# Performance work log

Measured on AMD Instinct MI355X. Metric: run time of the kernel, lower is better.

Reference implementation:

```python
import jax, jax.numpy as jnp
import numpy as np

B, S, D, N, R = 4, 2048, 1024, 64, 128

def setup_inputs() -> dict:
    key = jax.random.key(0)
    k1, k2, k3, k4, k5 = jax.random.split(key, 5)
    x = jax.random.normal(k1, (B, S, D), dtype=jnp.float32)
    feature_know_w = jax.random.uniform(k2, (B, S, N), dtype=jnp.float32)
    restore_know_w = jax.random.uniform(k3, (B, S, N), dtype=jnp.float32)
    # neuron pools, scaled like typical init
    feature_know = jax.random.normal(k4, (N, D, R), dtype=jnp.float32) / np.sqrt(D)
    restore_know = jax.random.normal(k5, (N, R, D), dtype=jnp.float32) / np.sqrt(R)
    return {"x": x, "feature_know_w": feature_know_w, "restore_know_w": restore_know_w,
            "feature_know": feature_know, "restore_know": restore_know}

def reference(x, feature_know_w, restore_know_w, feature_know, restore_know):
    # Feature stage: all_h[b,s,n,r] = sum_d x[b,s,d] * feature_know[n,d,r];
    # h[b,s,r] = sum_n all_h[b,s,n,r] * feature_know_w[b,s,n].
    # Fused into one einsum (same math, XLA picks pairwise contraction;
    # largest intermediate is [B,S,N,R], never [B,S,N,D]).
    h = jnp.einsum('bsd,ndr,bsn->bsr', x, feature_know, feature_know_w)
    # Restore stage: all_out[b,s,n,d] = sum_r h[b,s,r] * restore_know[n,r,d];
    # out[b,s,d] = sum_n all_out[b,s,n,d] * restore_know_w[b,s,n].
    # Reordered contraction keeps the intermediate at [B,S,N,R] instead of [B,S,N,D].
    out = jnp.einsum('bsr,bsn,nrd->bsd', h, restore_know_w, restore_know)
    # dropout p=0.0 -> identity
    return out
```

## Files before the change

### kernel.cpp

```cpp
#include <hip/hip_runtime.h>
#include <stdint.h>


typedef unsigned short ushort_t;
typedef __attribute__((ext_vector_type(8))) short frag_t;
typedef __attribute__((ext_vector_type(4))) float f32x4;

#define BK 128

__device__ __forceinline__ unsigned short f2bf(float f) {
    unsigned int u = __builtin_bit_cast(unsigned int, f);
    u = (u + 0x7FFFu + ((u >> 16) & 1u)) >> 16;
    return (unsigned short)u;
}

__device__ __forceinline__ void glds16(const ushort_t* g, ushort_t* l) {
    __builtin_amdgcn_global_load_lds(
        (const __attribute__((address_space(1))) unsigned int*)g,
        (__attribute__((address_space(3))) unsigned int*)l,
        16, 0, 0);
}

__global__ __launch_bounds__(256) void convert_bf(const float* __restrict__ in,
                                                  ushort_t* __restrict__ out, int n8) {
    int idx = blockIdx.x * 256 + threadIdx.x;
    if (idx >= n8) return;
    const float4 v0 = ((const float4*)in)[idx * 2];
    const float4 v1 = ((const float4*)in)[idx * 2 + 1];
    unsigned short b[8] = { f2bf(v0.x), f2bf(v0.y), f2bf(v0.z), f2bf(v0.w),
                            f2bf(v1.x), f2bf(v1.y), f2bf(v1.z), f2bf(v1.w) };
    ((uint4*)out)[idx] = *(const uint4*)b;
}

__global__ __launch_bounds__(256) void transpose_bf(const float* __restrict__ in,
                                                    ushort_t* __restrict__ out,
                                                    int R, int C) {
    __shared__ float tile[64][65];
    const int t  = threadIdx.x;
    const int r0 = blockIdx.x * 64;
    const int c0 = blockIdx.y * 64;
    const int ci = t & 63;
    const int rb = t >> 6;
    #pragma unroll
    for (int p = 0; p < 16; ++p)
        tile[rb + 4 * p][ci] = in[(size_t)(r0 + rb + 4 * p) * C + c0 + ci];
    __syncthreads();
    const int cw = t >> 2;
    const int rg = (t & 3) * 16;
    unsigned short buf[16];
    #pragma unroll
    for (int k = 0; k < 16; ++k)
        buf[k] = f2bf(tile[rg + k][cw]);
    uint4* dst = (uint4*)&out[(size_t)(c0 + cw) * R + r0 + rg];
    dst[0] = *(const uint4*)&buf[0];
    dst[1] = *(const uint4*)&buf[8];
}

template<int SHIFT, int SEG_STEPS, bool ATOMIC>
__global__ __launch_bounds__(256, 2)
void kc_gemm(const ushort_t* __restrict__ Ab, const float* __restrict__ W,
             const ushort_t* __restrict__ Bt, float* __restrict__ C,
             int ldA, int ldB, int ldC, int ksteps)
{
    __shared__ ushort_t As[128 * BK];
    __shared__ ushort_t Bs[128 * BK];

    const int t    = threadIdx.x;
    const int lane = t & 63;
    const int wv   = t >> 6;
    const int m0   = blockIdx.x * 128;
    const int n0   = blockIdx.y * 128;
    const int kbase = blockIdx.z * ksteps * BK;

    const int wm = (wv & 1) * 64;
    const int wn = (wv >> 1) * 64;
    const int fr = lane & 15;
    const int q  = lane >> 4;

    int srow[8], scol[8];
    #pragma unroll
    for (int c = 0; c < 8; ++c) {
        const int s = (wv * 8 + c) * 64 + lane;
        srow[c] = s >> 4;
        scol[c] = ((s & 15) ^ (srow[c] & 15)) * 8;
    }

    f32x4 acc_out[4][4], acc_in[4][4];
    #pragma unroll
    for (int i = 0; i < 4; ++i)
        #pragma unroll
        for (int j = 0; j < 4; ++j)
            acc_out[i][j] = (f32x4){0.f, 0.f, 0.f, 0.f};

    const int nsegs = ksteps / SEG_STEPS;
    for (int seg = 0; seg < nsegs; ++seg) {
        const int segk = kbase + seg * SEG_STEPS * BK;
        const int nidx = segk >> SHIFT;

        #pragma unroll
        for (int i = 0; i < 4; ++i)
            #pragma unroll
            for (int j = 0; j < 4; ++j)
                acc_in[i][j] = (f32x4){0.f, 0.f, 0.f, 0.f};

        for (int ss = 0; ss < SEG_STEPS; ++ss) {
            const int k0 = segk + ss * BK;
            const int d0 = k0 & ((1 << SHIFT) - 1);

            __syncthreads();
            #pragma unroll
            for (int c = 0; c < 8; ++c) {
                glds16(Ab + (size_t)(m0 + srow[c]) * ldA + d0 + scol[c],
                       &As[(wv * 8 + c) * 512]);
                glds16(Bt + (size_t)(n0 + srow[c]) * ldB + k0 + scol[c],
                       &Bs[(wv * 8 + c) * 512]);
            }
            __syncthreads();

            #pragma unroll
            for (int kk = 0; kk < 4; ++kk) {
                frag_t a[4], b[4];
                const int csw = (q + 4 * kk) ^ fr;
                #pragma unroll
                for (int i = 0; i < 4; ++i) {
                    a[i] = *(const frag_t*)&As[((wm + 16 * i + fr) * 16 + csw) * 8];
                    b[i] = *(const frag_t*)&Bs[((wn + 16 * i + fr) * 16 + csw) * 8];
                }
                #pragma unroll
                for (int i = 0; i < 4; ++i)
                    #pragma unroll
                    for (int j = 0; j < 4; ++j)
                        acc_in[i][j] = __builtin_amdgcn_mfma_f32_16x16x32_bf16(
                                           a[i], b[j], acc_in[i][j], 0, 0, 0);
            }
        }

        #pragma unroll
        for (int i = 0; i < 4; ++i) {
            #pragma unroll
            for (int r = 0; r < 4; ++r) {
                const int gm = m0 + wm + 16 * i + q * 4 + r;
                const float w = W[(size_t)gm * 64 + nidx];
                #pragma unroll
                for (int j = 0; j < 4; ++j)
                    acc_out[i][j][r] += w * acc_in[i][j][r];
            }
        }
    }

    #pragma unroll
    for (int i = 0; i < 4; ++i) {
        #pragma unroll
        for (int j = 0; j < 4; ++j) {
            #pragma unroll
            for (int r = 0; r < 4; ++r) {
                const int gm = m0 + wm + 16 * i + q * 4 + r;
                const int gn = n0 + wn + 16 * j + fr;
                if constexpr (ATOMIC)
                    atomicAdd(&C[(size_t)gm * ldC + gn], acc_out[i][j][r]);
                else
                    C[(size_t)gm * ldC + gn] = acc_out[i][j][r];
            }
        }
    }
}

extern "C" void kernel_launch(void* const* d_in, const int* in_sizes, int n_in,
                              void* d_out, int out_size, void* d_ws, size_t ws_size,
                              hipStream_t stream) {
    const float* x  = (const float*)d_in[0];
    const float* w1 = (const float*)d_in[1];
    const float* w2 = (const float*)d_in[2];
    const float* F  = (const float*)d_in[3];
    const float* Rk = (const float*)d_in[4];
    float* out = (float*)d_out;

    char* ws = (char*)d_ws;
    float*    h    = (float*)ws;
    ushort_t* buf1 = (ushort_t*)(ws + ((size_t)4  << 20));
    ushort_t* F_t  = (ushort_t*)(ws + ((size_t)20 << 20));
    ushort_t* h_bf = (ushort_t*)(ws + ((size_t)36 << 20));

    hipMemsetAsync(h, 0, (size_t)8192 * 128 * sizeof(float), stream);

    convert_bf<<<4096, 256, 0, stream>>>(x, buf1, 1048576);
    transpose_bf<<<dim3(1024, 2), 256, 0, stream>>>(F, F_t, 65536, 128);

    kc_gemm<10, 8, true><<<dim3(64, 1, 8), 256, 0, stream>>>(
        buf1, w1, F_t, h, 1024, 65536, 128, 64);

    convert_bf<<<512, 256, 0, stream>>>(h, h_bf, 131072);
    transpose_bf<<<dim3(128, 16), 256, 0, stream>>>(Rk, buf1, 8192, 1024);

    kc_gemm<7, 1, false><<<dim3(64, 8, 1), 256, 0, stream>>>(
        h_bf, w2, buf1, out, 128, 8192, 1024, 64);
}
```

Before: 497.0 us.

## Shrink GEMM tile to 64x128 with BK=64 to raise occupancy and block count

Shrinks the GEMM block tile from 128x128 with BK=128 to 64x128 with BK=64. LDS shrinks and per-wave accumulators halve, so the launch bound rises to 4 blocks per CU. The grids double in the M dimension and the K-step and segment counts are rescaled to match, with a new XOR swizzle for the 8-chunk rows. The goal is more resident waves and more blocks to hide latency across the CUs. In exchange, each tile reuses its loads less, adds more barrier round-trips per unit of work, and the feature GEMM issues more atomics.

```diff
diff --git a/kernel.cpp b/kernel.cpp
--- a/kernel.cpp
+++ b/kernel.cpp
@@ -6,7 +6,7 @@
 typedef __attribute__((ext_vector_type(8))) short frag_t;
 typedef __attribute__((ext_vector_type(4))) float f32x4;
 
-#define BK 128
+#define BK 64
 
 __device__ __forceinline__ unsigned short f2bf(float f) {
     unsigned int u = __builtin_bit_cast(unsigned int, f);
@@ -57,37 +57,45 @@
 }
 
 template<int SHIFT, int SEG_STEPS, bool ATOMIC>
-__global__ __launch_bounds__(256, 2)
+__global__ __launch_bounds__(256, 4)
 void kc_gemm(const ushort_t* __restrict__ Ab, const float* __restrict__ W,
              const ushort_t* __restrict__ Bt, float* __restrict__ C,
              int ldA, int ldB, int ldC, int ksteps)
 {
-    __shared__ ushort_t As[128 * BK];
+    __shared__ ushort_t As[64 * BK];
     __shared__ ushort_t Bs[128 * BK];
 
     const int t    = threadIdx.x;
     const int lane = t & 63;
     const int wv   = t >> 6;
-    const int m0   = blockIdx.x * 128;
+    const int m0   = blockIdx.x * 64;
     const int n0   = blockIdx.y * 128;
     const int kbase = blockIdx.z * ksteps * BK;
 
-    const int wm = (wv & 1) * 64;
+    const int wm = (wv & 1) * 32;
     const int wn = (wv >> 1) * 64;
     const int fr = lane & 15;
     const int q  = lane >> 4;
-
-    int srow[8], scol[8];
-    #pragma unroll
-    for (int c = 0; c < 8; ++c) {
-        const int s = (wv * 8 + c) * 64 + lane;
-        srow[c] = s >> 4;
-        scol[c] = ((s & 15) ^ (srow[c] & 15)) * 8;
-    }
-
-    f32x4 acc_out[4][4], acc_in[4][4];
-    #pragma unroll
-    for (int i = 0; i < 4; ++i)
+    const int e  = fr & 7;
+
+    int arow[2], acol[2];
+    #pragma unroll
+    for (int c = 0; c < 2; ++c) {
+        const int s = (wv * 2 + c) * 64 + lane;
+        arow[c] = s >> 3;
+        acol[c] = ((s & 7) ^ (arow[c] & 7)) * 8;
+    }
+    int brow[4], bcol[4];
+    #pragma unroll
+    for (int c = 0; c < 4; ++c) {
+        const int s = (wv * 4 + c) * 64 + lane;
+        brow[c] = s >> 3;
+        bcol[c] = ((s & 7) ^ (brow[c] & 7)) * 8;
+    }
+
+    f32x4 acc_out[2][4];
+    #pragma unroll
+    for (int i = 0; i < 2; ++i)
         #pragma unroll
         for (int j = 0; j < 4; ++j)
             acc_out[i][j] = (f32x4){0.f, 0.f, 0.f, 0.f};
@@ -97,8 +105,9 @@
         const int segk = kbase + seg * SEG_STEPS * BK;
         const int nidx = segk >> SHIFT;
 
-        #pragma unroll
-        for (int i = 0; i < 4; ++i)
+        f32x4 acc_in[2][4];
+        #pragma unroll
+        for (int i = 0; i < 2; ++i)
             #pragma unroll
             for (int j = 0; j < 4; ++j)
                 acc_in[i][j] = (f32x4){0.f, 0.f, 0.f, 0.f};
@@ -109,25 +118,27 @@
 
             __syncthreads();
             #pragma unroll
-            for (int c = 0; c < 8; ++c) {
-                glds16(Ab + (size_t)(m0 + srow[c]) * ldA + d0 + scol[c],
-                       &As[(wv * 8 + c) * 512]);
-                glds16(Bt + (size_t)(n0 + srow[c]) * ldB + k0 + scol[c],
-                       &Bs[(wv * 8 + c) * 512]);
-            }
+            for (int c = 0; c < 2; ++c)
+                glds16(Ab + (size_t)(m0 + arow[c]) * ldA + d0 + acol[c],
+                       &As[(wv * 2 + c) * 512]);
+            #pragma unroll
+            for (int c = 0; c < 4; ++c)
+                glds16(Bt + (size_t)(n0 + brow[c]) * ldB + k0 + bcol[c],
+                       &Bs[(wv * 4 + c) * 512]);
             __syncthreads();
 
             #pragma unroll
-            for (int kk = 0; kk < 4; ++kk) {
-                frag_t a[4], b[4];
-                const int csw = (q + 4 * kk) ^ fr;
-                #pragma unroll
-                for (int i = 0; i < 4; ++i) {
-                    a[i] = *(const frag_t*)&As[((wm + 16 * i + fr) * 16 + csw) * 8];
-                    b[i] = *(const frag_t*)&Bs[((wn + 16 * i + fr) * 16 + csw) * 8];
-                }
-                #pragma unroll
-                for (int i = 0; i < 4; ++i)
+            for (int kk = 0; kk < 2; ++kk) {
+                const int csw = (kk * 4 + q) ^ e;
+                frag_t a[2], b[4];
+                #pragma unroll
+                for (int i = 0; i < 2; ++i)
+                    a[i] = *(const frag_t*)&As[((wm + 16 * i + fr) * 8 + csw) * 8];
+                #pragma unroll
+                for (int j = 0; j < 4; ++j)
+                    b[j] = *(const frag_t*)&Bs[((wn + 16 * j + fr) * 8 + csw) * 8];
+                #pragma unroll
+                for (int i = 0; i < 2; ++i)
                     #pragma unroll
                     for (int j = 0; j < 4; ++j)
                         acc_in[i][j] = __builtin_amdgcn_mfma_f32_16x16x32_bf16(
@@ -136,7 +147,7 @@
         }
 
         #pragma unroll
-        for (int i = 0; i < 4; ++i) {
+        for (int i = 0; i < 2; ++i) {
             #pragma unroll
             for (int r = 0; r < 4; ++r) {
                 const int gm = m0 + wm + 16 * i + q * 4 + r;
@@ -149,7 +160,7 @@
     }
 
     #pragma unroll
-    for (int i = 0; i < 4; ++i) {
+    for (int i = 0; i < 2; ++i) {
         #pragma unroll
         for (int j = 0; j < 4; ++j) {
             #pragma unroll
@@ -186,12 +197,12 @@
     convert_bf<<<4096, 256, 0, stream>>>(x, buf1, 1048576);
     transpose_bf<<<dim3(1024, 2), 256, 0, stream>>>(F, F_t, 65536, 128);
 
-    kc_gemm<10, 8, true><<<dim3(64, 1, 8), 256, 0, stream>>>(
-        buf1, w1, F_t, h, 1024, 65536, 128, 64);
+    kc_gemm<10, 16, true><<<dim3(128, 1, 8), 256, 0, stream>>>(
+        buf1, w1, F_t, h, 1024, 65536, 128, 128);
 
     convert_bf<<<512, 256, 0, stream>>>(h, h_bf, 131072);
     transpose_bf<<<dim3(128, 16), 256, 0, stream>>>(Rk, buf1, 8192, 1024);
 
-    kc_gemm<7, 1, false><<<dim3(64, 8, 1), 256, 0, stream>>>(
-        h_bf, w2, buf1, out, 128, 8192, 1024, 64);
-}
+    kc_gemm<7, 2, false><<<dim3(128, 8, 1), 256, 0, stream>>>(
+        h_bf, w2, buf1, out, 128, 8192, 1024, 128);
+}
```

New measurement: 500.4 us. No clear change (+0.7%).

## Split feature GEMM per neuron and pre-scale restore input into a dense g matrix

Applied to the files above, without the earlier changes.

The feature GEMM now splits across all 64 neurons in the grid z dimension. Each block scales its tile by the routing weight and atomically adds into h, replacing the in-register segment accumulation. When the workspace is large enough, a new make_g kernel writes w2-scaled h into a 8192x8192 bf16 matrix so the restore stage becomes a plain GEMM; otherwise it falls back to a per-neuron split with atomics. BK drops to 64 and the occupancy hint rises to 3. The trade is much more atomic traffic into h and a large extra g buffer written and read back, in exchange for simpler inner loops and more parallel blocks.

```diff
diff --git a/kernel.cpp b/kernel.cpp
--- a/kernel.cpp
+++ b/kernel.cpp
@@ -6,7 +6,7 @@
 typedef __attribute__((ext_vector_type(8))) short frag_t;
 typedef __attribute__((ext_vector_type(4))) float f32x4;
 
-#define BK 128
+#define BK 64
 
 __device__ __forceinline__ unsigned short f2bf(float f) {
     unsigned int u = __builtin_bit_cast(unsigned int, f);
@@ -56,11 +56,27 @@
     dst[1] = *(const uint4*)&buf[8];
 }
 
-template<int SHIFT, int SEG_STEPS, bool ATOMIC>
-__global__ __launch_bounds__(256, 2)
-void kc_gemm(const ushort_t* __restrict__ Ab, const float* __restrict__ W,
-             const ushort_t* __restrict__ Bt, float* __restrict__ C,
-             int ldA, int ldB, int ldC, int ksteps)
+__global__ __launch_bounds__(256) void make_g(const float* __restrict__ h,
+                                              const float* __restrict__ w2,
+                                              ushort_t* __restrict__ g) {
+    const int idx = blockIdx.x * 256 + threadIdx.x;
+    const int m  = idx >> 10;
+    const int c  = idx & 1023;
+    const int n  = c >> 4;
+    const int r0 = (c & 15) * 8;
+    const float w = w2[m * 64 + n];
+    const float4 h0 = *(const float4*)(h + (size_t)m * 128 + r0);
+    const float4 h1 = *(const float4*)(h + (size_t)m * 128 + r0 + 4);
+    unsigned short b[8] = { f2bf(w * h0.x), f2bf(w * h0.y), f2bf(w * h0.z), f2bf(w * h0.w),
+                            f2bf(w * h1.x), f2bf(w * h1.y), f2bf(w * h1.z), f2bf(w * h1.w) };
+    ((uint4*)g)[idx] = *(const uint4*)b;
+}
+
+template<bool SPLITN>
+__global__ __launch_bounds__(256, 3)
+void kc_gemm(const ushort_t* __restrict__ Ab, const ushort_t* __restrict__ Bt,
+             const float* __restrict__ W, float* __restrict__ C,
+             int ldA, int ldB, int ldC, int ksteps, int b_seg)
 {
     __shared__ ushort_t As[128 * BK];
     __shared__ ushort_t Bs[128 * BK];
@@ -70,96 +86,78 @@
     const int wv   = t >> 6;
     const int m0   = blockIdx.x * 128;
     const int n0   = blockIdx.y * 128;
-    const int kbase = blockIdx.z * ksteps * BK;
+    const int nz   = SPLITN ? blockIdx.z : 0;
+    const size_t bko = (size_t)nz * b_seg;
 
     const int wm = (wv & 1) * 64;
     const int wn = (wv >> 1) * 64;
     const int fr = lane & 15;
     const int q  = lane >> 4;
-
-    int srow[8], scol[8];
-    #pragma unroll
-    for (int c = 0; c < 8; ++c) {
-        const int s = (wv * 8 + c) * 64 + lane;
-        srow[c] = s >> 4;
-        scol[c] = ((s & 15) ^ (srow[c] & 15)) * 8;
-    }
-
-    f32x4 acc_out[4][4], acc_in[4][4];
+    const int e  = fr & 7;
+
+    int srow[4], scol[4];
+    #pragma unroll
+    for (int c = 0; c < 4; ++c) {
+        const int s = (wv * 4 + c) * 64 + lane;
+        srow[c] = s >> 3;
+        scol[c] = ((s & 7) ^ (srow[c] & 7)) * 8;
+    }
+
+    f32x4 acc[4][4];
     #pragma unroll
     for (int i = 0; i < 4; ++i)
         #pragma unroll
         for (int j = 0; j < 4; ++j)
-            acc_out[i][j] = (f32x4){0.f, 0.f, 0.f, 0.f};
-
-    const int nsegs = ksteps / SEG_STEPS;
-    for (int seg = 0; seg < nsegs; ++seg) {
-        const int segk = kbase + seg * SEG_STEPS * BK;
-        const int nidx = segk >> SHIFT;
-
-        #pragma unroll
-        for (int i = 0; i < 4; ++i)
+            acc[i][j] = (f32x4){0.f, 0.f, 0.f, 0.f};
+
+    for (int ss = 0; ss < ksteps; ++ss) {
+        const int k0 = ss * BK;
+
+        __syncthreads();
+        #pragma unroll
+        for (int c = 0; c < 4; ++c)
+            glds16(Ab + (size_t)(m0 + srow[c]) * ldA + k0 + scol[c],
+                   &As[(wv * 4 + c) * 512]);
+        #pragma unroll
+        for (int c = 0; c < 4; ++c)
+            glds16(Bt + (size_t)(n0 + srow[c]) * ldB + bko + k0 + scol[c],
+                   &Bs[(wv * 4 + c) * 512]);
+        __syncthreads();
+
+        #pragma unroll
+        for (int kk = 0; kk < 2; ++kk) {
+            const int csw = (kk * 4 + q) ^ e;
+            frag_t a[4], b[4];
+            #pragma unroll
+            for (int i = 0; i < 4; ++i)
+                a[i] = *(const frag_t*)&As[((wm + 16 * i + fr) * 8 + csw) * 8];
             #pragma unroll
             for (int j = 0; j < 4; ++j)
-                acc_in[i][j] = (f32x4){0.f, 0.f, 0.f, 0.f};
-
-        for (int ss = 0; ss < SEG_STEPS; ++ss) {
-            const int k0 = segk + ss * BK;
-            const int d0 = k0 & ((1 << SHIFT) - 1);
-
-            __syncthreads();
+                b[j] = *(const frag_t*)&Bs[((wn + 16 * j + fr) * 8 + csw) * 8];
             #pragma unroll
-            for (int c = 0; c < 8; ++c) {
-                glds16(Ab + (size_t)(m0 + srow[c]) * ldA + d0 + scol[c],
-                       &As[(wv * 8 + c) * 512]);
-                glds16(Bt + (size_t)(n0 + srow[c]) * ldB + k0 + scol[c],
-                       &Bs[(wv * 8 + c) * 512]);
-            }
-            __syncthreads();
-
-            #pragma unroll
-            for (int kk = 0; kk < 4; ++kk) {
-                frag_t a[4], b[4];
-                const int csw = (q + 4 * kk) ^ fr;
-                #pragma unroll
-                for (int i = 0; i < 4; ++i) {
-                    a[i] = *(const frag_t*)&As[((wm + 16 * i + fr) * 16 + csw) * 8];
-                    b[i] = *(const frag_t*)&Bs[((wn + 16 * i + fr) * 16 + csw) * 8];
-                }
-                #pragma unroll
-                for (int i = 0; i < 4; ++i)
-                    #pragma unroll
-                    for (int j = 0; j < 4; ++j)
-                        acc_in[i][j] = __builtin_amdgcn_mfma_f32_16x16x32_bf16(
-                                           a[i], b[j], acc_in[i][j], 0, 0, 0);
-            }
-        }
-
-        #pragma unroll
-        for (int i = 0; i < 4; ++i) {
-            #pragma unroll
-            for (int r = 0; r < 4; ++r) {
-                const int gm = m0 + wm + 16 * i + q * 4 + r;
-                const float w = W[(size_t)gm * 64 + nidx];
+            for (int i = 0; i < 4; ++i)
                 #pragma unroll
                 for (int j = 0; j < 4; ++j)
-                    acc_out[i][j][r] += w * acc_in[i][j][r];
-            }
+                    acc[i][j] = __builtin_amdgcn_mfma_f32_16x16x32_bf16(
+                                    a[i], b[j], acc[i][j], 0, 0, 0);
         }
     }
 
     #pragma unroll
     for (int i = 0; i < 4; ++i) {
         #pragma unroll
-        for (int j = 0; j < 4; ++j) {
-            #pragma unroll
-            for (int r = 0; r < 4; ++r) {
-                const int gm = m0 + wm + 16 * i + q * 4 + r;
-                const int gn = n0 + wn + 16 * j + fr;
-                if constexpr (ATOMIC)
-                    atomicAdd(&C[(size_t)gm * ldC + gn], acc_out[i][j][r]);
-                else
-                    C[(size_t)gm * ldC + gn] = acc_out[i][j][r];
+        for (int r = 0; r < 4; ++r) {
+            const int gm = m0 + wm + 16 * i + q * 4 + r;
+            if constexpr (SPLITN) {
+                const float w = W[(size_t)gm * 64 + nz];
+                #pragma unroll
+                for (int j = 0; j < 4; ++j)
+                    atomicAdd(&C[(size_t)gm * ldC + n0 + wn + 16 * j + fr],
+                              w * acc[i][j][r]);
+            } else {
+                #pragma unroll
+                for (int j = 0; j < 4; ++j)
+                    C[(size_t)gm * ldC + n0 + wn + 16 * j + fr] = acc[i][j][r];
             }
         }
     }
@@ -176,22 +174,46 @@
     float* out = (float*)d_out;
 
     char* ws = (char*)d_ws;
-    float*    h    = (float*)ws;
-    ushort_t* buf1 = (ushort_t*)(ws + ((size_t)4  << 20));
-    ushort_t* F_t  = (ushort_t*)(ws + ((size_t)20 << 20));
-    ushort_t* h_bf = (ushort_t*)(ws + ((size_t)36 << 20));
-
-    hipMemsetAsync(h, 0, (size_t)8192 * 128 * sizeof(float), stream);
-
-    convert_bf<<<4096, 256, 0, stream>>>(x, buf1, 1048576);
-    transpose_bf<<<dim3(1024, 2), 256, 0, stream>>>(F, F_t, 65536, 128);
-
-    kc_gemm<10, 8, true><<<dim3(64, 1, 8), 256, 0, stream>>>(
-        buf1, w1, F_t, h, 1024, 65536, 128, 64);
-
-    convert_bf<<<512, 256, 0, stream>>>(h, h_bf, 131072);
-    transpose_bf<<<dim3(128, 16), 256, 0, stream>>>(Rk, buf1, 8192, 1024);
-
-    kc_gemm<7, 1, false><<<dim3(64, 8, 1), 256, 0, stream>>>(
-        h_bf, w2, buf1, out, 128, 8192, 1024, 64);
-}
+    const size_t MB = (size_t)1 << 20;
+
+    if (ws_size >= 148 * MB) {
+        float*    h    = (float*)ws;
+        ushort_t* x_bf = (ushort_t*)(ws + 4   * MB);
+        ushort_t* F_t  = (ushort_t*)(ws + 20  * MB);
+        ushort_t* g    = (ushort_t*)(ws + 4   * MB);
+        ushort_t* Rk_t = (ushort_t*)(ws + 132 * MB);
+
+        hipMemsetAsync(h, 0, 4 * MB, stream);
+        convert_bf<<<4096, 256, 0, stream>>>(x, x_bf, 1048576);
+        transpose_bf<<<dim3(1024, 2), 256, 0, stream>>>(F, F_t, 65536, 128);
+        transpose_bf<<<dim3(128, 16), 256, 0, stream>>>(Rk, Rk_t, 8192, 1024);
+
+        kc_gemm<true><<<dim3(64, 1, 64), 256, 0, stream>>>(
+            x_bf, F_t, w1, h, 1024, 65536, 128, 16, 1024);
+
+        make_g<<<32768, 256, 0, stream>>>(h, w2, g);
+
+        kc_gemm<false><<<dim3(64, 8, 1), 256, 0, stream>>>(
+            g, Rk_t, nullptr, out, 8192, 8192, 1024, 128, 0);
+    } else {
+        float*    h    = (float*)ws;
+        ushort_t* x_bf = (ushort_t*)(ws + 4  * MB);
+        ushort_t* Rk_t = (ushort_t*)(ws + 4  * MB);
+        ushort_t* F_t  = (ushort_t*)(ws + 20 * MB);
+        ushort_t* h_bf = (ushort_t*)(ws + 36 * MB);
+
+        hipMemsetAsync(h, 0, 4 * MB, stream);
+        hipMemsetAsync(out, 0, (size_t)8192 * 1024 * sizeof(float), stream);
+        convert_bf<<<4096, 256, 0, stream>>>(x, x_bf, 1048576);
+        transpose_bf<<<dim3(1024, 2), 256, 0, stream>>>(F, F_t, 65536, 128);
+
+        kc_gemm<true><<<dim3(64, 1, 64), 256, 0, stream>>>(
+            x_bf, F_t, w1, h, 1024, 65536, 128, 16, 1024);
+
+        convert_bf<<<512, 256, 0, stream>>>(h, h_bf, 131072);
+        transpose_bf<<<dim3(128, 16), 256, 0, stream>>>(Rk, Rk_t, 8192, 1024);
+
+        kc_gemm<true><<<dim3(64, 8, 64), 256, 0, stream>>>(
+            h_bf, Rk_t, w2, out, 128, 8192, 1024, 2, 128);
+    }
+}
```

Result: slower. 559.7 us (+12.6%).
